# Kernel tuning notes

Hardware: AMD Instinct MI355X
Metric: run time of the kernel (lower is better)

Reference implementation:

```python
import jax, jax.numpy as jnp
import numpy as np

SCALE_REACH = 10.0   # 'scale' in forward
SCALE_COS = 16.0     # CosNorm_Classifier default scale


def setup_inputs() -> dict:
    key = jax.random.key(0)
    ks = jax.random.split(key, 7)
    B, C, F = 64, 1000, 2048
    return {
        "x": jax.random.normal(ks[0], (B, F), jnp.float32),
        "centroids": jax.random.normal(ks[1], (C, F), jnp.float32),
        "W_hall": jax.random.normal(ks[2], (C, F), jnp.float32) * 0.02,
        "b_hall": jax.random.normal(ks[3], (C,), jnp.float32) * 0.02,
        "W_sel": jax.random.normal(ks[4], (F, F), jnp.float32) * 0.02,
        "b_sel": jax.random.normal(ks[5], (F,), jnp.float32) * 0.02,
        "W_cos": jax.random.normal(ks[6], (C, F), jnp.float32) * 0.001,
    }


def reference(x, centroids, W_hall, b_hall, W_sel, b_sel, W_cos):
    direct_feature = x
    # L2 distance to every class centroid: [B, C] (materializes [B, C, F] diff as in torch)
    diff = x[:, None, :] - centroids[None, :, :]
    dist = jnp.sqrt(jnp.sum(diff * diff, axis=2))
    # original sorts then takes column 0 -> min distance
    min_dist = jnp.min(dist, axis=1)                      # [B]
    reachability = (SCALE_REACH / min_dist)[:, None]      # [B, 1], broadcast over feat

    # hallucinated memory read
    values_memory = jax.nn.softmax(x @ W_hall.T + b_hall, axis=1)  # [B, C]
    memory_feature = values_memory @ centroids                      # [B, F]

    concept_selector = jnp.tanh(x @ W_sel.T + b_sel)                # [B, F]
    infused_feature = concept_selector * memory_feature
    feat = reachability * (direct_feature + infused_feature)

    # CosNorm classifier
    norm_x = jnp.linalg.norm(feat, axis=1, keepdims=True)           # [B, 1]
    ex = (norm_x / (1.0 + norm_x)) * (feat / norm_x)                # norm-gated unit vec
    ew = W_cos / jnp.linalg.norm(W_cos, axis=1, keepdims=True)      # [C, F]
    logits = ex @ (ew.T * SCALE_COS)                                # [B, C]

    return logits, direct_feature, infused_feature
```

## Files before the change

### kernel.cpp

```cpp
#include <hip/hip_runtime.h>
#include <math.h>

#define FF 2048

typedef __attribute__((ext_vector_type(8))) short short8;
typedef __attribute__((ext_vector_type(4))) float floatx4;

#define OFF_SPART 0
#define OFF_HPART 1024000
#define OFF_SELP  2048000
#define OFF_MEMP  3096576
#define OFF_LOGP  5193728
#define OFF_HROW  7241728
#define OFF_FEAT  7307264
#define OFF_CN2   7438336
#define OFF_WINV  7439336
#define OFF_XN2   7440336
#define OFF_MM    7440400
#define OFF_ROWF  7442448
#define OFF_NRM2P 7442704
#define OFF_CTR   7443216
#define OFF_FLAG  7444240

#define TP 40

__device__ __forceinline__ float cld(const float* p) {
  return __hip_atomic_load(p, __ATOMIC_RELAXED, __HIP_MEMORY_SCOPE_AGENT);
}
__device__ __forceinline__ void cst(float* p, float v) {
  __hip_atomic_store(p, v, __ATOMIC_RELAXED, __HIP_MEMORY_SCOPE_AGENT);
}
__device__ __forceinline__ floatx4 cld4(const float* p) {
  floatx4 d;
  asm volatile("global_load_dwordx4 %0, %1, off sc0 sc1\n\ts_waitcnt vmcnt(0)"
               : "=&v"(d) : "v"(p) : "memory");
  return d;
}
__device__ __forceinline__ void cld4x4(const float* p0, const float* p1,
                                       const float* p2, const float* p3,
                                       floatx4& a, floatx4& b, floatx4& c, floatx4& d) {
  asm volatile(
      "global_load_dwordx4 %0, %4, off sc0 sc1\n\t"
      "global_load_dwordx4 %1, %5, off sc0 sc1\n\t"
      "global_load_dwordx4 %2, %6, off sc0 sc1\n\t"
      "global_load_dwordx4 %3, %7, off sc0 sc1\n\t"
      "s_waitcnt vmcnt(0)"
      : "=&v"(a), "=&v"(b), "=&v"(c), "=&v"(d)
      : "v"(p0), "v"(p1), "v"(p2), "v"(p3)
      : "memory");
}
__device__ __forceinline__ void cst4(float* p, floatx4 v) {
  asm volatile("global_store_dwordx4 %0, %1, off sc0 sc1" :: "v"(p), "v"(v) : "memory");
}

__device__ __forceinline__ void split2(float f, ushort& h, ushort& l) {
  unsigned u = __float_as_uint(f);
  float r = f - __uint_as_float(u & 0xffff0000u);
  h = (ushort)(u >> 16);
  l = (ushort)(__float_as_uint(r) >> 16);
}

__device__ __forceinline__ void stage_bt_bf(const float* __restrict__ M, int ldK, int rowBase,
                                            int nrows, int k0, int kmax,
                                            ushort* __restrict__ hi, ushort* __restrict__ lo, int t) {
  int r = t >> 2, q = t & 3;
  int grow = rowBase + r;
  bool rok = grow < nrows;
  const float* src = M + (size_t)grow * ldK + k0 + q * 8;
#pragma unroll
  for (int h = 0; h < 2; ++h) {
    int kb = k0 + q * 8 + h * 4;
    float4 v = make_float4(0.f, 0.f, 0.f, 0.f);
    if (rok) {
      if (kb + 3 < kmax) {
        v = *(const float4*)(src + h * 4);
      } else {
#pragma unroll
        for (int j = 0; j < 4; ++j)
          if (kb + j < kmax) ((float*)&v)[j] = src[h * 4 + j];
      }
    }
    ushort4 hv, lv;
    split2(v.x, hv.x, lv.x); split2(v.y, hv.y, lv.y);
    split2(v.z, hv.z, lv.z); split2(v.w, hv.w, lv.w);
    int base = r * TP + q * 8 + h * 4;
    *(ushort4*)(hi + base) = hv;
    *(ushort4*)(lo + base) = lv;
  }
}

__device__ __forceinline__ void stage_v(const float* __restrict__ hrowg, float gm, float inv,
                                        int k0, ushort* __restrict__ hi, ushort* __restrict__ lo, int t) {
  int r = t >> 2, q = t & 3;
#pragma unroll
  for (int h = 0; h < 2; ++h) {
    int kb = k0 + q * 8 + h * 4;
    floatx4 hv4 = cld4(hrowg + (size_t)r * 1024 + kb);
    float v[4];
#pragma unroll
    for (int j = 0; j < 4; ++j)
      v[j] = (kb + j < 1000) ? expf(hv4[j] - gm) * inv : 0.f;
    ushort4 hv, lv;
    split2(v[0], hv.x, lv.x); split2(v[1], hv.y, lv.y);
    split2(v[2], hv.z, lv.z); split2(v[3], hv.w, lv.w);
    int base = r * TP + q * 8 + h * 4;
    *(ushort4*)(hi + base) = hv;
    *(ushort4*)(lo + base) = lv;
  }
}

__device__ __forceinline__ void stage_feat4(const float* __restrict__ feat, int k0,
                                            ushort* __restrict__ hi, ushort* __restrict__ lo, int t) {
  int r = t >> 2, q = t & 3;
#pragma unroll
  for (int h = 0; h < 2; ++h) {
    floatx4 v = cld4(feat + (size_t)r * 2048 + k0 + q * 8 + h * 4);
    ushort4 hv, lv;
    split2(v[0], hv.x, lv.x); split2(v[1], hv.y, lv.y);
    split2(v[2], hv.z, lv.z); split2(v[3], hv.w, lv.w);
    int base = r * TP + q * 8 + h * 4;
    *(ushort4*)(hi + base) = hv;
    *(ushort4*)(lo + base) = lv;
  }
}

__device__ __forceinline__ void stage_tr_bf(const float* __restrict__ M, int ldN, int k0, int kmax,
                                            int n0, ushort* __restrict__ hi, ushort* __restrict__ lo, int t) {
  int kk = t >> 3, c8 = (t & 7) * 8;
  int gk = k0 + kk;
  const float* src = M + (size_t)gk * ldN + n0 + c8;
  float4 v0 = make_float4(0.f, 0.f, 0.f, 0.f), v1 = v0;
  if (gk < kmax) { v0 = *(const float4*)src; v1 = *(const float4*)(src + 4); }
#pragma unroll
  for (int j = 0; j < 8; ++j) {
    float f = (j < 4) ? ((float*)&v0)[j] : ((float*)&v1)[j - 4];
    ushort h, l;
    split2(f, h, l);
    hi[(c8 + j) * TP + kk] = h;
    lo[(c8 + j) * TP + kk] = l;
  }
}

#define MFMA(a, b, c) __builtin_amdgcn_mfma_f32_16x16x32_bf16(a, b, c, 0, 0, 0)

#define NBLK 512

__device__ __forceinline__ void gbar(unsigned* __restrict__ ctr, unsigned* __restrict__ flag,
                                     unsigned phase) {
  asm volatile("s_waitcnt vmcnt(0)" ::: "memory");
  __syncthreads();
  int t = threadIdx.x;
  if (t == 0)
    __hip_atomic_fetch_add(ctr + (blockIdx.x & 63) * 16, 1u, __ATOMIC_RELAXED, __HIP_MEMORY_SCOPE_AGENT);
  if (blockIdx.x == 0) {
    if (t < 64) {
      unsigned target = (unsigned)NBLK * phase;
      for (;;) {
        unsigned v = __hip_atomic_load(ctr + t * 16, __ATOMIC_RELAXED, __HIP_MEMORY_SCOPE_AGENT);
#pragma unroll
        for (int off = 32; off > 0; off >>= 1) v += __shfl_down(v, off, 64);
        v = __shfl(v, 0, 64);
        if (v >= target) break;
        __builtin_amdgcn_s_sleep(1);
      }
      if (t == 0)
        __hip_atomic_store(flag + phase * 16, 1u, __ATOMIC_RELAXED, __HIP_MEMORY_SCOPE_AGENT);
    }
  } else {
    if (t == 0) {
      while (__hip_atomic_load(flag + phase * 16, __ATOMIC_RELAXED, __HIP_MEMORY_SCOPE_AGENT) == 0u)
        __builtin_amdgcn_s_sleep(2);
    }
  }
  __syncthreads();
}

__global__ void k_init(unsigned* ctr) {
  int t = threadIdx.x;
#pragma unroll
  for (int i = 0; i < 5; ++i)
    __hip_atomic_store(ctr + i * 256 + t, 0u, __ATOMIC_RELAXED, __HIP_MEMORY_SCOPE_AGENT);
}

__global__ __launch_bounds__(256) void k_all(
    const float* __restrict__ x, const float* __restrict__ cent,
    const float* __restrict__ whall, const float* __restrict__ bhall,
    const float* __restrict__ wsel, const float* __restrict__ bsel,
    const float* __restrict__ wcos, float* __restrict__ ws, float* __restrict__ out) {
  __shared__ __align__(16) char smem[6 * 64 * TP * 2];
  ushort* Ah  = (ushort*)smem;
  ushort* Al  = Ah + 64 * TP;
  ushort* B1h = Ah + 2 * 64 * TP;
  ushort* B1l = Ah + 3 * 64 * TP;
  ushort* B2h = Ah + 4 * 64 * TP;
  ushort* B2l = Ah + 5 * 64 * TP;
  float* red2 = (float*)smem;

  int bx = blockIdx.x, t = threadIdx.x;
  int lane = t & 63, w = t >> 6;
  int ln15 = t & 15, lq = (t >> 4) & 3, q8 = lq * 8;
  int mh = w & 1, nh = w >> 1;
  unsigned* ctr  = (unsigned*)(ws + OFF_CTR);
  unsigned* flag = (unsigned*)(ws + OFF_FLAG);

  for (int r = bx * 4 + w; r < 2064; r += 2048) {
    const float* src = (r < 1000) ? cent + (size_t)r * FF
                     : (r < 2000) ? wcos + (size_t)(r - 1000) * FF
                                  : x + (size_t)(r - 2000) * FF;
    float s = 0.f;
#pragma unroll
    for (int i = 0; i < 8; ++i) {
      float4 v = *(const float4*)(src + i * 256 + lane * 4);
      s += v.x * v.x + v.y * v.y + v.z * v.z + v.w * v.w;
    }
#pragma unroll
    for (int off = 32; off > 0; off >>= 1) s += __shfl_down(s, off, 64);
    if (lane == 0) {
      if (r < 1000) cst(ws + OFF_CN2 + r, s);
      else if (r < 2000) cst(ws + OFF_WINV + (r - 1000), 1.f / sqrtf(s));
      else cst(ws + OFF_XN2 + (r - 2000), s);
    }
  }

  if (bx < 256) {
    int tile = bx & 15, ks = bx >> 4;
    int n0 = tile * 64;
    floatx4 accS[2][2], accH[2][2];
#pragma unroll
    for (int i = 0; i < 2; ++i)
#pragma unroll
      for (int j = 0; j < 2; ++j) { accS[i][j] = (floatx4){0.f,0.f,0.f,0.f}; accH[i][j] = (floatx4){0.f,0.f,0.f,0.f}; }
    for (int kc = 0; kc < 4; ++kc) {
      int k0 = ks * 128 + kc * 32;
      __syncthreads();
      stage_bt_bf(x,     FF, 0,  64,   k0, FF, Ah,  Al,  t);
      stage_bt_bf(cent,  FF, n0, 1000, k0, FF, B1h, B1l, t);
      stage_bt_bf(whall, FF, n0, 1000, k0, FF, B2h, B2l, t);
      __syncthreads();
      short8 ah[2], al[2];
#pragma unroll
      for (int i = 0; i < 2; ++i) {
        int row = (mh * 2 + i) * 16 + ln15;
        ah[i] = *(const short8*)(Ah + row * TP + q8);
        al[i] = *(const short8*)(Al + row * TP + q8);
      }
#pragma unroll
      for (int j = 0; j < 2; ++j) {
        int brow = (nh * 2 + j) * 16 + ln15;
        short8 b1h = *(const short8*)(B1h + brow * TP + q8);
        short8 b1l = *(const short8*)(B1l + brow * TP + q8);
        short8 b2h = *(const short8*)(B2h + brow * TP + q8);
        short8 b2l = *(const short8*)(B2l + brow * TP + q8);
#pragma unroll
        for (int i = 0; i < 2; ++i) {
          accS[i][j] = MFMA(ah[i], b1h, accS[i][j]);
          accS[i][j] = MFMA(ah[i], b1l, accS[i][j]);
          accS[i][j] = MFMA(al[i], b1h, accS[i][j]);
          accH[i][j] = MFMA(ah[i], b2h, accH[i][j]);
          accH[i][j] = MFMA(ah[i], b2l, accH[i][j]);
          accH[i][j] = MFMA(al[i], b2h, accH[i][j]);
        }
      }
    }
    float* Spart = ws + OFF_SPART + (size_t)ks * 64000;
    float* Hpart = ws + OFF_HPART + (size_t)ks * 64000;
#pragma unroll
    for (int i = 0; i < 2; ++i)
#pragma unroll
      for (int j = 0; j < 2; ++j) {
        int gn = n0 + (nh * 2 + j) * 16 + ln15;
        if (gn < 1000) {
#pragma unroll
          for (int r = 0; r < 4; ++r) {
            int gm = (mh * 2 + i) * 16 + lq * 4 + r;
            cst(Spart + gm * 1000 + gn, accS[i][j][r]);
            cst(Hpart + gm * 1000 + gn, accH[i][j][r]);
          }
        }
      }
  } else {
    int b2 = bx - 256;
    int tile = b2 & 31, ks = b2 >> 5;
    int n0 = tile * 64;
    floatx4 acc[2][2];
#pragma unroll
    for (int i = 0; i < 2; ++i)
#pragma unroll
      for (int j = 0; j < 2; ++j) acc[i][j] = (floatx4){0.f,0.f,0.f,0.f};
    for (int kc = 0; kc < 8; ++kc) {
      int k0 = ks * 256 + kc * 32;
      __syncthreads();
      stage_bt_bf(x,    FF, 0,  64, k0, FF, Ah,  Al,  t);
      stage_bt_bf(wsel, FF, n0, FF, k0, FF, B1h, B1l, t);
      __syncthreads();
      short8 ah[2], al[2];
#pragma unroll
      for (int i = 0; i < 2; ++i) {
        int row = (mh * 2 + i) * 16 + ln15;
        ah[i] = *(const short8*)(Ah + row * TP + q8);
        al[i] = *(const short8*)(Al + row * TP + q8);
      }
#pragma unroll
      for (int j = 0; j < 2; ++j) {
        int brow = (nh * 2 + j) * 16 + ln15;
        short8 bh = *(const short8*)(B1h + brow * TP + q8);
        short8 bl = *(const short8*)(B1l + brow * TP + q8);
#pragma unroll
        for (int i = 0; i < 2; ++i) {
          acc[i][j] = MFMA(ah[i], bh, acc[i][j]);
          acc[i][j] = MFMA(ah[i], bl, acc[i][j]);
          acc[i][j] = MFMA(al[i], bh, acc[i][j]);
        }
      }
    }
    float* selp = ws + OFF_SELP + (size_t)ks * 131072;
#pragma unroll
    for (int i = 0; i < 2; ++i)
#pragma unroll
      for (int j = 0; j < 2; ++j) {
        int gn = n0 + (nh * 2 + j) * 16 + ln15;
#pragma unroll
        for (int r = 0; r < 4; ++r) {
          int gm = (mh * 2 + i) * 16 + lq * 4 + r;
          cst(selp + gm * 2048 + gn, acc[i][j][r]);
        }
      }
  }

  gbar(ctr, flag, 1);

  {
    int b = bx >> 3, ch = bx & 7;
    int g = t >> 5, ci = t & 31;
    int c = ch * 128 + ci * 4;
    const float* Sp  = ws + OFF_SPART + (size_t)g * 64000 + b * 1000 + c;
    const float* Hp  = ws + OFF_HPART + (size_t)g * 64000 + b * 1000 + c;
    floatx4 s1, s2, h1, h2;
    cld4x4(Sp, Sp + 8 * 64000, Hp, Hp + 8 * 64000, s1, s2, h1, h2);
    float S4[4], H4[4];
#pragma unroll
    for (int j = 0; j < 4; ++j) {
      S4[j] = s1[j] + s2[j];
      H4[j] = h1[j] + h2[j];
    }
#pragma unroll
    for (int j = 0; j < 4; ++j) {
      red2[(g * 32 + ci) * 8 + j]     = S4[j];
      red2[(g * 32 + ci) * 8 + 4 + j] = H4[j];
    }
    __syncthreads();
    if (t < 32) {
      float S[4] = {0,0,0,0}, H[4] = {0,0,0,0};
#pragma unroll
      for (int g2 = 0; g2 < 8; ++g2)
#pragma unroll
        for (int j = 0; j < 4; ++j) {
          S[j] += red2[(g2 * 32 + t) * 8 + j];
          H[j] += red2[(g2 * 32 + t) * 8 + 4 + j];
        }
      int c0 = ch * 128 + t * 4;
      float xn = cld(ws + OFF_XN2 + b);
      float Hf[4], lmin = 3.0e38f, lmax = -3.0e38f;
#pragma unroll
      for (int j = 0; j < 4; ++j) {
        bool valid = (c0 + j) < 1000;
        float bh = valid ? bhall[c0 + j] : 0.f;
        Hf[j] = valid ? (H[j] + bh) : -3.0e38f;
        float cn = valid ? cld(ws + OFF_CN2 + c0 + j) : 0.f;
        float d2 = valid ? (xn - 2.f * S[j] + cn) : 3.0e38f;
        lmin = fminf(lmin, d2);
        lmax = fmaxf(lmax, Hf[j]);
      }
      cst4(ws + OFF_HROW + b * 1024 + c0, (floatx4){Hf[0], Hf[1], Hf[2], Hf[3]});
      float cmin = lmin, cmax = lmax;
#pragma unroll
      for (int off = 16; off > 0; off >>= 1) {
        cmin = fminf(cmin, __shfl_down(cmin, off, 32));
        cmax = fmaxf(cmax, __shfl_down(cmax, off, 32));
      }
      cmin = __shfl(cmin, 0, 32);
      cmax = __shfl(cmax, 0, 32);
      float lsum = 0.f;
#pragma unroll
      for (int j = 0; j < 4; ++j)
        if ((c0 + j) < 1000) lsum += expf(Hf[j] - cmax);
#pragma unroll
      for (int off = 16; off > 0; off >>= 1) lsum += __shfl_down(lsum, off, 32);
      if (t == 0) {
        float* mm = ws + OFF_MM + (b * 8 + ch) * 4;
        cst(mm + 0, cmin);
        cst(mm + 1, cmax);
        cst(mm + 2, lsum);
      }
    }
  }

  gbar(ctr, flag, 2);

  if (bx < 64 && t < 8) {
    const float* mm = ws + OFF_MM + (bx * 8 + t) * 4;
    float mn = cld(mm + 0), mx = cld(mm + 1), sm = cld(mm + 2);
    float gmin = mn, gmax = mx;
#pragma unroll
    for (int off = 4; off > 0; off >>= 1) {
      gmin = fminf(gmin, __shfl_down(gmin, off, 8));
      gmax = fmaxf(gmax, __shfl_down(gmax, off, 8));
    }
    gmin = __shfl(gmin, 0, 8);
    gmax = __shfl(gmax, 0, 8);
    float dp = sm * expf(mx - gmax);
#pragma unroll
    for (int off = 4; off > 0; off >>= 1) dp += __shfl_down(dp, off, 8);
    if (t == 0) {
      float* rf = ws + OFF_ROWF + bx * 4;
      cst(rf + 0, gmax);
      cst(rf + 1, 1.f / dp);
      cst(rf + 2, 10.f / sqrtf(gmin));
    }
  }

  gbar(ctr, flag, 3);

  {
    int tile = bx & 31, ks = bx >> 5;
    int n0 = tile * 64;
    int vr = t >> 2;
    float gm  = cld(ws + OFF_ROWF + vr * 4 + 0);
    float inv = cld(ws + OFF_ROWF + vr * 4 + 1);
    floatx4 acc[2][2];
#pragma unroll
    for (int i = 0; i < 2; ++i)
#pragma unroll
      for (int j = 0; j < 2; ++j) acc[i][j] = (floatx4){0.f,0.f,0.f,0.f};
    for (int kc = 0; kc < 2; ++kc) {
      int k0 = ks * 64 + kc * 32;
      __syncthreads();
      stage_v(ws + OFF_HROW, gm, inv, k0, Ah, Al, t);
      stage_tr_bf(cent, FF, k0, 1000, n0, B1h, B1l, t);
      __syncthreads();
      short8 ah[2], al[2];
#pragma unroll
      for (int i = 0; i < 2; ++i) {
        int row = (mh * 2 + i) * 16 + ln15;
        ah[i] = *(const short8*)(Ah + row * TP + q8);
        al[i] = *(const short8*)(Al + row * TP + q8);
      }
#pragma unroll
      for (int j = 0; j < 2; ++j) {
        int brow = (nh * 2 + j) * 16 + ln15;
        short8 bh = *(const short8*)(B1h + brow * TP + q8);
        short8 bl = *(const short8*)(B1l + brow * TP + q8);
#pragma unroll
        for (int i = 0; i < 2; ++i) {
          acc[i][j] = MFMA(ah[i], bh, acc[i][j]);
          acc[i][j] = MFMA(ah[i], bl, acc[i][j]);
          acc[i][j] = MFMA(al[i], bh, acc[i][j]);
        }
      }
    }
    float* memp = ws + OFF_MEMP + (size_t)ks * 131072;
#pragma unroll
    for (int i = 0; i < 2; ++i)
#pragma unroll
      for (int j = 0; j < 2; ++j) {
        int gn = n0 + (nh * 2 + j) * 16 + ln15;
#pragma unroll
        for (int r = 0; r < 4; ++r) {
          int gm2 = (mh * 2 + i) * 16 + lq * 4 + r;
          cst(memp + gm2 * 2048 + gn, acc[i][j][r]);
        }
      }
  }

  gbar(ctr, flag, 4);

  if (t < 64) {
    int row = bx >> 3, ch2 = bx & 7;
    int f = ch2 * 256 + t * 4;
    const float* selp = ws + OFF_SELP + (size_t)row * 2048 + f;
    const float* memp = ws + OFF_MEMP + (size_t)row * 2048 + f;
    floatx4 a0, a1, a2, a3;
    float sp[4], mm4[4];
    cld4x4(selp, selp + 131072, selp + 2 * 131072, selp + 3 * 131072, a0, a1, a2, a3);
#pragma unroll
    for (int j = 0; j < 4; ++j)
      sp[j] = a0[j] + a1[j] + a2[j] + a3[j];
    cld4x4(selp + 4 * 131072, selp + 5 * 131072, selp + 6 * 131072, selp + 7 * 131072, a0, a1, a2, a3);
#pragma unroll
    for (int j = 0; j < 4; ++j)
      sp[j] += a0[j] + a1[j] + a2[j] + a3[j];
#pragma unroll
    for (int j = 0; j < 4; ++j) mm4[j] = 0.f;
#pragma unroll
    for (int q = 0; q < 4; ++q) {
      cld4x4(memp + (size_t)(4 * q) * 131072, memp + (size_t)(4 * q + 1) * 131072,
             memp + (size_t)(4 * q + 2) * 131072, memp + (size_t)(4 * q + 3) * 131072,
             a0, a1, a2, a3);
#pragma unroll
      for (int j = 0; j < 4; ++j)
        mm4[j] += a0[j] + a1[j] + a2[j] + a3[j];
    }
    float4 bs4 = *(const float4*)(bsel + f);
    float4 x4  = *(const float4*)(x + (size_t)row * 2048 + f);
    float rch = cld(ws + OFF_ROWF + row * 4 + 2);
    float4 inf4;
    floatx4 ft4;
    float nrm2 = 0.f;
#pragma unroll
    for (int j = 0; j < 4; ++j) {
      float sel = tanhf(sp[j] + ((float*)&bs4)[j]);
      float inf = sel * mm4[j];
      float ft = rch * (((float*)&x4)[j] + inf);
      ((float*)&inf4)[j] = inf;
      ft4[j] = ft;
      nrm2 += ft * ft;
    }
    *(float4*)(out + 64000 + (size_t)row * 2048 + f) = x4;
    *(float4*)(out + 195072 + (size_t)row * 2048 + f) = inf4;
    cst4(ws + OFF_FEAT + (size_t)row * 2048 + f, ft4);
#pragma unroll
    for (int off = 32; off > 0; off >>= 1) nrm2 += __shfl_down(nrm2, off, 64);
    if (t == 0) cst(ws + OFF_NRM2P + row * 8 + ch2, nrm2);
  }

  gbar(ctr, flag, 5);

  {
    int tile = bx & 15, ks = bx >> 4;
    int n0 = tile * 64;
    floatx4 acc[2][2];
#pragma unroll
    for (int i = 0; i < 2; ++i)
#pragma unroll
      for (int j = 0; j < 2; ++j) acc[i][j] = (floatx4){0.f,0.f,0.f,0.f};
    for (int kc = 0; kc < 2; ++kc) {
      int k0 = ks * 64 + kc * 32;
      __syncthreads();
      stage_feat4(ws + OFF_FEAT, k0, Ah, Al, t);
      stage_bt_bf(wcos, FF, n0, 1000, k0, FF, B1h, B1l, t);
      __syncthreads();
      short8 ah[2], al[2];
#pragma unroll
      for (int i = 0; i < 2; ++i) {
        int row = (mh * 2 + i) * 16 + ln15;
        ah[i] = *(const short8*)(Ah + row * TP + q8);
        al[i] = *(const short8*)(Al + row * TP + q8);
      }
#pragma unroll
      for (int j = 0; j < 2; ++j) {
        int brow = (nh * 2 + j) * 16 + ln15;
        short8 bh = *(const short8*)(B1h + brow * TP + q8);
        short8 bl = *(const short8*)(B1l + brow * TP + q8);
#pragma unroll
        for (int i = 0; i < 2; ++i) {
          acc[i][j] = MFMA(ah[i], bh, acc[i][j]);
          acc[i][j] = MFMA(ah[i], bl, acc[i][j]);
          acc[i][j] = MFMA(al[i], bh, acc[i][j]);
        }
      }
    }
    float* logp = ws + OFF_LOGP + (size_t)ks * 64000;
#pragma unroll
    for (int i = 0; i < 2; ++i)
#pragma unroll
      for (int j = 0; j < 2; ++j) {
        int gn = n0 + (nh * 2 + j) * 16 + ln15;
        if (gn < 1000) {
#pragma unroll
          for (int r = 0; r < 4; ++r) {
            int gm = (mh * 2 + i) * 16 + lq * 4 + r;
            cst(logp + gm * 1000 + gn, acc[i][j][r]);
          }
        }
      }
  }

  gbar(ctr, flag, 6);

  if (bx < 500 && t < 32) {
    int idx0 = (bx * 32 + t) * 4;
    const float* logp = ws + OFF_LOGP + idx0;
    float s4[4] = {0,0,0,0};
    floatx4 a0, a1, a2, a3;
#pragma unroll
    for (int q = 0; q < 8; ++q) {
      cld4x4(logp + (size_t)(4 * q) * 64000, logp + (size_t)(4 * q + 1) * 64000,
             logp + (size_t)(4 * q + 2) * 64000, logp + (size_t)(4 * q + 3) * 64000,
             a0, a1, a2, a3);
#pragma unroll
      for (int j = 0; j < 4; ++j)
        s4[j] += a0[j] + a1[j] + a2[j] + a3[j];
    }
    floatx4 o4;
    int pb = -1;
    float sfac = 0.f;
#pragma unroll
    for (int j = 0; j < 4; ++j) {
      int idx = idx0 + j;
      int bb = idx / 1000;
      int cc = idx - bb * 1000;
      if (bb != pb) {
        float n2 = 0.f;
#pragma unroll
        for (int q = 0; q < 8; ++q) n2 += cld(ws + OFF_NRM2P + bb * 8 + q);
        sfac = 16.f / (1.f + sqrtf(n2));
        pb = bb;
      }
      o4[j] = s4[j] * sfac * cld(ws + OFF_WINV + cc);
    }
    *(floatx4*)(out + idx0) = o4;
  }
}

extern "C" void kernel_launch(void* const* d_in, const int* in_sizes, int n_in,
                              void* d_out, int out_size, void* d_ws, size_t ws_size,
                              hipStream_t stream) {
  const float* x     = (const float*)d_in[0];
  const float* cent  = (const float*)d_in[1];
  const float* whall = (const float*)d_in[2];
  const float* bhall = (const float*)d_in[3];
  const float* wsel  = (const float*)d_in[4];
  const float* bsel  = (const float*)d_in[5];
  const float* wcos  = (const float*)d_in[6];
  float* out = (float*)d_out;
  float* ws  = (float*)d_ws;
  unsigned* ctr = (unsigned*)(ws + OFF_CTR);

  hipLaunchKernelGGL(k_init, dim3(1), dim3(256), 0, stream, ctr);
  hipLaunchKernelGGL(k_all, dim3(NBLK), dim3(256), 0, stream,
                     x, cent, whall, bhall, wsel, bsel, wcos, ws, out);
}
```

Measured before the change: 136.3 us.

## Double persistent grid to 1024 blocks and halve per-block split-K work

Raises the persistent cooperative kernel from 512 to 1024 blocks, with launch bounds set for 4 blocks per CU, and doubles the split-K factor in every GEMM phase so each block handles half the K range. The softmax, feature and logit reduction stages are repartitioned to match, with more partials, narrower per-block chunks and vectorised norm-partial loads. The goal is to fill more CUs and hide latency in these small-M GEMMs. In exchange the grid barriers must wait on twice as many blocks, the partial-sum workspace traffic doubles, and residency of all 1024 blocks at once is required to avoid deadlock.

```diff
diff --git a/kernel.cpp b/kernel.cpp
--- a/kernel.cpp
+++ b/kernel.cpp
@@ -7,20 +7,20 @@
 typedef __attribute__((ext_vector_type(4))) float floatx4;
 
 #define OFF_SPART 0
-#define OFF_HPART 1024000
-#define OFF_SELP  2048000
-#define OFF_MEMP  3096576
-#define OFF_LOGP  5193728
-#define OFF_HROW  7241728
-#define OFF_FEAT  7307264
-#define OFF_CN2   7438336
-#define OFF_WINV  7439336
-#define OFF_XN2   7440336
-#define OFF_MM    7440400
-#define OFF_ROWF  7442448
-#define OFF_NRM2P 7442704
-#define OFF_CTR   7443216
-#define OFF_FLAG  7444240
+#define OFF_HPART 2048000
+#define OFF_SELP  4096000
+#define OFF_MEMP  6193152
+#define OFF_LOGP  10387456
+#define OFF_HROW  14483456
+#define OFF_FEAT  14548992
+#define OFF_CN2   14680064
+#define OFF_WINV  14681064
+#define OFF_XN2   14682064
+#define OFF_MM    14682128
+#define OFF_ROWF  14686224
+#define OFF_NRM2P 14686480
+#define OFF_CTR   14687504
+#define OFF_FLAG  14688528
 
 #define TP 40
 
@@ -143,7 +143,7 @@
 
 #define MFMA(a, b, c) __builtin_amdgcn_mfma_f32_16x16x32_bf16(a, b, c, 0, 0, 0)
 
-#define NBLK 512
+#define NBLK 1024
 
 __device__ __forceinline__ void gbar(unsigned* __restrict__ ctr, unsigned* __restrict__ flag,
                                      unsigned phase) {
@@ -182,7 +182,7 @@
     __hip_atomic_store(ctr + i * 256 + t, 0u, __ATOMIC_RELAXED, __HIP_MEMORY_SCOPE_AGENT);
 }
 
-__global__ __launch_bounds__(256) void k_all(
+__global__ __launch_bounds__(256, 4) void k_all(
     const float* __restrict__ x, const float* __restrict__ cent,
     const float* __restrict__ whall, const float* __restrict__ bhall,
     const float* __restrict__ wsel, const float* __restrict__ bsel,
@@ -203,26 +203,29 @@
   unsigned* ctr  = (unsigned*)(ws + OFF_CTR);
   unsigned* flag = (unsigned*)(ws + OFF_FLAG);
 
-  for (int r = bx * 4 + w; r < 2064; r += 2048) {
-    const float* src = (r < 1000) ? cent + (size_t)r * FF
-                     : (r < 2000) ? wcos + (size_t)(r - 1000) * FF
-                                  : x + (size_t)(r - 2000) * FF;
-    float s = 0.f;
-#pragma unroll
-    for (int i = 0; i < 8; ++i) {
-      float4 v = *(const float4*)(src + i * 256 + lane * 4);
-      s += v.x * v.x + v.y * v.y + v.z * v.z + v.w * v.w;
-    }
-#pragma unroll
-    for (int off = 32; off > 0; off >>= 1) s += __shfl_down(s, off, 64);
-    if (lane == 0) {
-      if (r < 1000) cst(ws + OFF_CN2 + r, s);
-      else if (r < 2000) cst(ws + OFF_WINV + (r - 1000), 1.f / sqrtf(s));
-      else cst(ws + OFF_XN2 + (r - 2000), s);
-    }
-  }
-
-  if (bx < 256) {
+  {
+    int r = bx * 4 + w;
+    if (r < 2064) {
+      const float* src = (r < 1000) ? cent + (size_t)r * FF
+                       : (r < 2000) ? wcos + (size_t)(r - 1000) * FF
+                                    : x + (size_t)(r - 2000) * FF;
+      float s = 0.f;
+#pragma unroll
+      for (int i = 0; i < 8; ++i) {
+        float4 v = *(const float4*)(src + i * 256 + lane * 4);
+        s += v.x * v.x + v.y * v.y + v.z * v.z + v.w * v.w;
+      }
+#pragma unroll
+      for (int off = 32; off > 0; off >>= 1) s += __shfl_down(s, off, 64);
+      if (lane == 0) {
+        if (r < 1000) cst(ws + OFF_CN2 + r, s);
+        else if (r < 2000) cst(ws + OFF_WINV + (r - 1000), 1.f / sqrtf(s));
+        else cst(ws + OFF_XN2 + (r - 2000), s);
+      }
+    }
+  }
+
+  if (bx < 512) {
     int tile = bx & 15, ks = bx >> 4;
     int n0 = tile * 64;
     floatx4 accS[2][2], accH[2][2];
@@ -230,8 +233,8 @@
     for (int i = 0; i < 2; ++i)
 #pragma unroll
       for (int j = 0; j < 2; ++j) { accS[i][j] = (floatx4){0.f,0.f,0.f,0.f}; accH[i][j] = (floatx4){0.f,0.f,0.f,0.f}; }
-    for (int kc = 0; kc < 4; ++kc) {
-      int k0 = ks * 128 + kc * 32;
+    for (int kc = 0; kc < 2; ++kc) {
+      int k0 = ks * 64 + kc * 32;
       __syncthreads();
       stage_bt_bf(x,     FF, 0,  64,   k0, FF, Ah,  Al,  t);
       stage_bt_bf(cent,  FF, n0, 1000, k0, FF, B1h, B1l, t);
@@ -279,7 +282,7 @@
         }
       }
   } else {
-    int b2 = bx - 256;
+    int b2 = bx - 512;
     int tile = b2 & 31, ks = b2 >> 5;
     int n0 = tile * 64;
     floatx4 acc[2][2];
@@ -287,8 +290,8 @@
     for (int i = 0; i < 2; ++i)
 #pragma unroll
       for (int j = 0; j < 2; ++j) acc[i][j] = (floatx4){0.f,0.f,0.f,0.f};
-    for (int kc = 0; kc < 8; ++kc) {
-      int k0 = ks * 256 + kc * 32;
+    for (int kc = 0; kc < 4; ++kc) {
+      int k0 = ks * 128 + kc * 32;
       __syncthreads();
       stage_bt_bf(x,    FF, 0,  64, k0, FF, Ah,  Al,  t);
       stage_bt_bf(wsel, FF, n0, FF, k0, FF, B1h, B1l, t);
@@ -330,35 +333,31 @@
   gbar(ctr, flag, 1);
 
   {
-    int b = bx >> 3, ch = bx & 7;
-    int g = t >> 5, ci = t & 31;
-    int c = ch * 128 + ci * 4;
-    const float* Sp  = ws + OFF_SPART + (size_t)g * 64000 + b * 1000 + c;
-    const float* Hp  = ws + OFF_HPART + (size_t)g * 64000 + b * 1000 + c;
+    int b = bx >> 4, ch = bx & 15;
+    int g = t >> 4, c4 = (t & 15) * 4;
+    int c = ch * 64 + c4;
+    size_t base = (size_t)b * 1000 + c;
+    const float* Sp = ws + OFF_SPART + base;
+    const float* Hp = ws + OFF_HPART + base;
     floatx4 s1, s2, h1, h2;
-    cld4x4(Sp, Sp + 8 * 64000, Hp, Hp + 8 * 64000, s1, s2, h1, h2);
-    float S4[4], H4[4];
+    cld4x4(Sp + (size_t)(2 * g) * 64000, Sp + (size_t)(2 * g + 1) * 64000,
+           Hp + (size_t)(2 * g) * 64000, Hp + (size_t)(2 * g + 1) * 64000, s1, s2, h1, h2);
 #pragma unroll
     for (int j = 0; j < 4; ++j) {
-      S4[j] = s1[j] + s2[j];
-      H4[j] = h1[j] + h2[j];
-    }
-#pragma unroll
-    for (int j = 0; j < 4; ++j) {
-      red2[(g * 32 + ci) * 8 + j]     = S4[j];
-      red2[(g * 32 + ci) * 8 + 4 + j] = H4[j];
+      red2[(g * 16 + (t & 15)) * 8 + j]     = s1[j] + s2[j];
+      red2[(g * 16 + (t & 15)) * 8 + 4 + j] = h1[j] + h2[j];
     }
     __syncthreads();
-    if (t < 32) {
+    if (t < 16) {
       float S[4] = {0,0,0,0}, H[4] = {0,0,0,0};
 #pragma unroll
-      for (int g2 = 0; g2 < 8; ++g2)
+      for (int g2 = 0; g2 < 16; ++g2)
 #pragma unroll
         for (int j = 0; j < 4; ++j) {
-          S[j] += red2[(g2 * 32 + t) * 8 + j];
-          H[j] += red2[(g2 * 32 + t) * 8 + 4 + j];
+          S[j] += red2[(g2 * 16 + t) * 8 + j];
+          H[j] += red2[(g2 * 16 + t) * 8 + 4 + j];
         }
-      int c0 = ch * 128 + t * 4;
+      int c0 = ch * 64 + t * 4;
       float xn = cld(ws + OFF_XN2 + b);
       float Hf[4], lmin = 3.0e38f, lmax = -3.0e38f;
 #pragma unroll
@@ -374,20 +373,20 @@
       cst4(ws + OFF_HROW + b * 1024 + c0, (floatx4){Hf[0], Hf[1], Hf[2], Hf[3]});
       float cmin = lmin, cmax = lmax;
 #pragma unroll
-      for (int off = 16; off > 0; off >>= 1) {
-        cmin = fminf(cmin, __shfl_down(cmin, off, 32));
-        cmax = fmaxf(cmax, __shfl_down(cmax, off, 32));
-      }
-      cmin = __shfl(cmin, 0, 32);
-      cmax = __shfl(cmax, 0, 32);
+      for (int off = 8; off > 0; off >>= 1) {
+        cmin = fminf(cmin, __shfl_down(cmin, off, 16));
+        cmax = fmaxf(cmax, __shfl_down(cmax, off, 16));
+      }
+      cmin = __shfl(cmin, 0, 16);
+      cmax = __shfl(cmax, 0, 16);
       float lsum = 0.f;
 #pragma unroll
       for (int j = 0; j < 4; ++j)
         if ((c0 + j) < 1000) lsum += expf(Hf[j] - cmax);
 #pragma unroll
-      for (int off = 16; off > 0; off >>= 1) lsum += __shfl_down(lsum, off, 32);
+      for (int off = 8; off > 0; off >>= 1) lsum += __shfl_down(lsum, off, 16);
       if (t == 0) {
-        float* mm = ws + OFF_MM + (b * 8 + ch) * 4;
+        float* mm = ws + OFF_MM + (b * 16 + ch) * 4;
         cst(mm + 0, cmin);
         cst(mm + 1, cmax);
         cst(mm + 2, lsum);
@@ -397,20 +396,20 @@
 
   gbar(ctr, flag, 2);
 
-  if (bx < 64 && t < 8) {
-    const float* mm = ws + OFF_MM + (bx * 8 + t) * 4;
+  if (bx < 64 && t < 16) {
+    const float* mm = ws + OFF_MM + (bx * 16 + t) * 4;
     float mn = cld(mm + 0), mx = cld(mm + 1), sm = cld(mm + 2);
     float gmin = mn, gmax = mx;
 #pragma unroll
-    for (int off = 4; off > 0; off >>= 1) {
-      gmin = fminf(gmin, __shfl_down(gmin, off, 8));
-      gmax = fmaxf(gmax, __shfl_down(gmax, off, 8));
-    }
-    gmin = __shfl(gmin, 0, 8);
-    gmax = __shfl(gmax, 0, 8);
+    for (int off = 8; off > 0; off >>= 1) {
+      gmin = fminf(gmin, __shfl_down(gmin, off, 16));
+      gmax = fmaxf(gmax, __shfl_down(gmax, off, 16));
+    }
+    gmin = __shfl(gmin, 0, 16);
+    gmax = __shfl(gmax, 0, 16);
     float dp = sm * expf(mx - gmax);
 #pragma unroll
-    for (int off = 4; off > 0; off >>= 1) dp += __shfl_down(dp, off, 8);
+    for (int off = 8; off > 0; off >>= 1) dp += __shfl_down(dp, off, 16);
     if (t == 0) {
       float* rf = ws + OFF_ROWF + bx * 4;
       cst(rf + 0, gmax);
@@ -424,6 +423,7 @@
   {
     int tile = bx & 31, ks = bx >> 5;
     int n0 = tile * 64;
+    int k0 = ks * 32;
     int vr = t >> 2;
     float gm  = cld(ws + OFF_ROWF + vr * 4 + 0);
     float inv = cld(ws + OFF_ROWF + vr * 4 + 1);
@@ -432,30 +432,26 @@
     for (int i = 0; i < 2; ++i)
 #pragma unroll
       for (int j = 0; j < 2; ++j) acc[i][j] = (floatx4){0.f,0.f,0.f,0.f};
-    for (int kc = 0; kc < 2; ++kc) {
-      int k0 = ks * 64 + kc * 32;
-      __syncthreads();
-      stage_v(ws + OFF_HROW, gm, inv, k0, Ah, Al, t);
-      stage_tr_bf(cent, FF, k0, 1000, n0, B1h, B1l, t);
-      __syncthreads();
-      short8 ah[2], al[2];
+    stage_v(ws + OFF_HROW, gm, inv, k0, Ah, Al, t);
+    stage_tr_bf(cent, FF, k0, 1000, n0, B1h, B1l, t);
+    __syncthreads();
+    short8 ah[2], al[2];
+#pragma unroll
+    for (int i = 0; i < 2; ++i) {
+      int row = (mh * 2 + i) * 16 + ln15;
+      ah[i] = *(const short8*)(Ah + row * TP + q8);
+      al[i] = *(const short8*)(Al + row * TP + q8);
+    }
+#pragma unroll
+    for (int j = 0; j < 2; ++j) {
+      int brow = (nh * 2 + j) * 16 + ln15;
+      short8 bh = *(const short8*)(B1h + brow * TP + q8);
+      short8 bl = *(const short8*)(B1l + brow * TP + q8);
 #pragma unroll
       for (int i = 0; i < 2; ++i) {
-        int row = (mh * 2 + i) * 16 + ln15;
-        ah[i] = *(const short8*)(Ah + row * TP + q8);
-        al[i] = *(const short8*)(Al + row * TP + q8);
-      }
-#pragma unroll
-      for (int j = 0; j < 2; ++j) {
-        int brow = (nh * 2 + j) * 16 + ln15;
-        short8 bh = *(const short8*)(B1h + brow * TP + q8);
-        short8 bl = *(const short8*)(B1l + brow * TP + q8);
-#pragma unroll
-        for (int i = 0; i < 2; ++i) {
-          acc[i][j] = MFMA(ah[i], bh, acc[i][j]);
-          acc[i][j] = MFMA(ah[i], bl, acc[i][j]);
-          acc[i][j] = MFMA(al[i], bh, acc[i][j]);
-        }
+        acc[i][j] = MFMA(ah[i], bh, acc[i][j]);
+        acc[i][j] = MFMA(ah[i], bl, acc[i][j]);
+        acc[i][j] = MFMA(al[i], bh, acc[i][j]);
       }
     }
     float* memp = ws + OFF_MEMP + (size_t)ks * 131072;
@@ -474,25 +470,26 @@
 
   gbar(ctr, flag, 4);
 
-  if (t < 64) {
-    int row = bx >> 3, ch2 = bx & 7;
-    int f = ch2 * 256 + t * 4;
+  if (t < 32) {
+    int row = bx >> 4, ch2 = bx & 15;
+    int f = ch2 * 128 + t * 4;
     const float* selp = ws + OFF_SELP + (size_t)row * 2048 + f;
     const float* memp = ws + OFF_MEMP + (size_t)row * 2048 + f;
     floatx4 a0, a1, a2, a3;
     float sp[4], mm4[4];
-    cld4x4(selp, selp + 131072, selp + 2 * 131072, selp + 3 * 131072, a0, a1, a2, a3);
-#pragma unroll
-    for (int j = 0; j < 4; ++j)
-      sp[j] = a0[j] + a1[j] + a2[j] + a3[j];
-    cld4x4(selp + 4 * 131072, selp + 5 * 131072, selp + 6 * 131072, selp + 7 * 131072, a0, a1, a2, a3);
-#pragma unroll
-    for (int j = 0; j < 4; ++j)
-      sp[j] += a0[j] + a1[j] + a2[j] + a3[j];
-#pragma unroll
-    for (int j = 0; j < 4; ++j) mm4[j] = 0.f;
+#pragma unroll
+    for (int j = 0; j < 4; ++j) { sp[j] = 0.f; mm4[j] = 0.f; }
 #pragma unroll
     for (int q = 0; q < 4; ++q) {
+      cld4x4(selp + (size_t)(4 * q) * 131072, selp + (size_t)(4 * q + 1) * 131072,
+             selp + (size_t)(4 * q + 2) * 131072, selp + (size_t)(4 * q + 3) * 131072,
+             a0, a1, a2, a3);
+#pragma unroll
+      for (int j = 0; j < 4; ++j)
+        sp[j] += a0[j] + a1[j] + a2[j] + a3[j];
+    }
+#pragma unroll
+    for (int q = 0; q < 8; ++q) {
       cld4x4(memp + (size_t)(4 * q) * 131072, memp + (size_t)(4 * q + 1) * 131072,
              memp + (size_t)(4 * q + 2) * 131072, memp + (size_t)(4 * q + 3) * 131072,
              a0, a1, a2, a3);
@@ -519,8 +516,8 @@
     *(float4*)(out + 195072 + (size_t)row * 2048 + f) = inf4;
     cst4(ws + OFF_FEAT + (size_t)row * 2048 + f, ft4);
 #pragma unroll
-    for (int off = 32; off > 0; off >>= 1) nrm2 += __shfl_down(nrm2, off, 64);
-    if (t == 0) cst(ws + OFF_NRM2P + row * 8 + ch2, nrm2);
+    for (int off = 16; off > 0; off >>= 1) nrm2 += __shfl_down(nrm2, off, 32);
+    if (t == 0) cst(ws + OFF_NRM2P + row * 16 + ch2, nrm2);
   }
 
   gbar(ctr, flag, 5);
@@ -528,35 +525,32 @@
   {
     int tile = bx & 15, ks = bx >> 4;
     int n0 = tile * 64;
+    int k0 = ks * 32;
     floatx4 acc[2][2];
 #pragma unroll
     for (int i = 0; i < 2; ++i)
 #pragma unroll
       for (int j = 0; j < 2; ++j) acc[i][j] = (floatx4){0.f,0.f,0.f,0.f};
-    for (int kc = 0; kc < 2; ++kc) {
-      int k0 = ks * 64 + kc * 32;
-      __syncthreads();
-      stage_feat4(ws + OFF_FEAT, k0, Ah, Al, t);
-      stage_bt_bf(wcos, FF, n0, 1000, k0, FF, B1h, B1l, t);
-      __syncthreads();
-      short8 ah[2], al[2];
+    stage_feat4(ws + OFF_FEAT, k0, Ah, Al, t);
+    stage_bt_bf(wcos, FF, n0, 1000, k0, FF, B1h, B1l, t);
+    __syncthreads();
+    short8 ah[2], al[2];
+#pragma unroll
+    for (int i = 0; i < 2; ++i) {
+      int row = (mh * 2 + i) * 16 + ln15;
+      ah[i] = *(const short8*)(Ah + row * TP + q8);
+      al[i] = *(const short8*)(Al + row * TP + q8);
+    }
+#pragma unroll
+    for (int j = 0; j < 2; ++j) {
+      int brow = (nh * 2 + j) * 16 + ln15;
+      short8 bh = *(const short8*)(B1h + brow * TP + q8);
+      short8 bl = *(const short8*)(B1l + brow * TP + q8);
 #pragma unroll
       for (int i = 0; i < 2; ++i) {
-        int row = (mh * 2 + i) * 16 + ln15;
-        ah[i] = *(const short8*)(Ah + row * TP + q8);
-        al[i] = *(const short8*)(Al + row * TP + q8);
-      }
-#pragma unroll
-      for (int j = 0; j < 2; ++j) {
-        int brow = (nh * 2 + j) * 16 + ln15;
-        short8 bh = *(const short8*)(B1h + brow * TP + q8);
-        short8 bl = *(const short8*)(B1l + brow * TP + q8);
-#pragma unroll
-        for (int i = 0; i < 2; ++i) {
-          acc[i][j] = MFMA(ah[i], bh, acc[i][j]);
-          acc[i][j] = MFMA(ah[i], bl, acc[i][j]);
-          acc[i][j] = MFMA(al[i], bh, acc[i][j]);
-        }
+        acc[i][j] = MFMA(ah[i], bh, acc[i][j]);
+        acc[i][j] = MFMA(ah[i], bl, acc[i][j]);
+        acc[i][j] = MFMA(al[i], bh, acc[i][j]);
       }
     }
     float* logp = ws + OFF_LOGP + (size_t)ks * 64000;
@@ -583,7 +577,7 @@
     float s4[4] = {0,0,0,0};
     floatx4 a0, a1, a2, a3;
 #pragma unroll
-    for (int q = 0; q < 8; ++q) {
+    for (int q = 0; q < 16; ++q) {
       cld4x4(logp + (size_t)(4 * q) * 64000, logp + (size_t)(4 * q + 1) * 64000,
              logp + (size_t)(4 * q + 2) * 64000, logp + (size_t)(4 * q + 3) * 64000,
              a0, a1, a2, a3);
@@ -600,9 +594,12 @@
       int bb = idx / 1000;
       int cc = idx - bb * 1000;
       if (bb != pb) {
+        cld4x4(ws + OFF_NRM2P + bb * 16, ws + OFF_NRM2P + bb * 16 + 4,
+               ws + OFF_NRM2P + bb * 16 + 8, ws + OFF_NRM2P + bb * 16 + 12,
+               a0, a1, a2, a3);
         float n2 = 0.f;
 #pragma unroll
-        for (int q = 0; q < 8; ++q) n2 += cld(ws + OFF_NRM2P + bb * 8 + q);
+        for (int jj = 0; jj < 4; ++jj) n2 += a0[jj] + a1[jj] + a2[jj] + a3[jj];
         sfac = 16.f / (1.f + sqrtf(n2));
         pb = bb;
       }
```

Result: slower. 180.9 us (+32.7%).
